# Optimization experiments

Hardware: AMD Instinct MI355X
Metric: run time of the kernel (lower is better)

## Reference

```python
import jax, jax.numpy as jnp
import numpy as np

EPS = 1e-5
ROPE_BASE = 10000.0

def _rms_norm(x, alpha):
    # var = eps + mean(x^2) (eps added to mean, matching _rms_norm)
    var = EPS + jnp.mean(x * x, axis=-1, keepdims=True)
    return x * (alpha * jax.lax.rsqrt(var))

def _rope(x, pos):
    # x: [B,H,T,D], pos: [T] absolute positions; interleaved pair rotation
    D = x.shape[-1]
    half = D // 2
    inv_freq = ROPE_BASE ** (-jnp.arange(half, dtype=x.dtype) / half)
    ang = pos.astype(x.dtype)[:, None] * inv_freq[None, :]          # [T,half]
    cos, sin = jnp.cos(ang), jnp.sin(ang)
    x1, x2 = x[..., ::2], x[..., 1::2]
    y1 = x1 * cos - x2 * sin
    y2 = x1 * sin + x2 * cos
    return jnp.stack([y1, y2], axis=-1).reshape(x.shape)

def setup_inputs() -> dict:
    key = jax.random.key(0)
    ks = jax.random.split(key, 9)
    B, T, C = 8, 256, 2048
    H, Dh, CAP, FF = 16, 128, 2048, 8192
    s = 0.02
    return {
        "x": jax.random.normal(ks[0], (B, T, C), jnp.float32),
        "kcache": jax.random.normal(ks[1], (B, H, CAP, Dh), jnp.float32) * s,
        "vcache": jax.random.normal(ks[2], (B, H, CAP, Dh), jnp.float32) * s,
        "in_proj_w": jax.random.normal(ks[3], (3 * C, C), jnp.float32) * s,
        "out_proj_w": jax.random.normal(ks[4], (C, C), jnp.float32) * s,
        "norm1_a": jnp.ones((C,), jnp.float32),
        "norm2_a": jnp.ones((C,), jnp.float32),
        "w1": jax.random.normal(ks[5], (FF, C), jnp.float32) * s,
        "w2": jax.random.normal(ks[6], (C, FF), jnp.float32) * s,
        "offset": 1024,
    }

def reference(x, kcache, vcache, in_proj_w, out_proj_w, norm1_a, norm2_a, w1, w2, offset):
    B, T, C = x.shape
    H = 16
    Dh = C // H
    CAP = kcache.shape[2]
    scale = 1.0 / np.sqrt(Dh)

    # ---- self-attention branch ----
    xn = _rms_norm(x, norm1_a)
    qkv = jnp.einsum('btc,oc->bto', xn, in_proj_w)                  # [B,T,3C]
    q, k, v = jnp.split(qkv, 3, axis=-1)
    def heads(t):  # [B,T,C] -> [B,H,T,Dh]
        return t.reshape(B, T, H, Dh).transpose(0, 2, 1, 3)
    q, k, v = heads(q), heads(k), heads(v)

    t_abs = offset + jnp.arange(T)                                   # absolute positions
    q = _rope(q, t_abs)
    k = _rope(k, t_abs)

    # ---- ring KV cache write: idx = (offset + t) % capacity ----
    widx = (offset + jnp.arange(T)) % CAP                            # [T]
    kcache = kcache.at[:, :, widx, :].set(k)
    vcache = vcache.at[:, :, widx, :].set(v)

    # ---- recover absolute positions of cache slots (RingKVCache.complete) ----
    idx = jnp.arange(CAP)
    last = offset + T - 1
    end_index = last % CAP
    delta = idx - end_index
    pos = jnp.where(delta <= 0, last + delta, last + delta - CAP)    # [CAP]
    invalid = idx >= (offset + T)
    pos = jnp.where(invalid, -1, pos)

    # ---- causal + context masked attention over full cache ----
    qpos = offset + jnp.arange(T)                                    # [T]
    d = qpos[:, None] - pos[None, :]                                 # [T,CAP]
    mask = (pos[None, :] >= 0) & (d >= 0) & (d < CAP)
    scores = jnp.einsum('bhtd,bhsd->bhts', q, kcache) * scale        # [B,H,T,CAP]
    scores = jnp.where(mask[None, None], scores, jnp.float32(-1e9))
    attn = jax.nn.softmax(scores, axis=-1)
    o = jnp.einsum('bhts,bhsd->bhtd', attn, vcache)                  # [B,H,T,Dh]
    o = o.transpose(0, 2, 1, 3).reshape(B, T, C)
    x = x + jnp.einsum('btc,oc->bto', o, out_proj_w)

    # ---- MLP branch ----
    h = _rms_norm(x, norm2_a)
    h = jax.nn.gelu(jnp.einsum('btc,fc->btf', h, w1), approximate=False)
    x = x + jnp.einsum('btf,cf->btc', h, w2)
    return x
```

## Files before the change

kernel.cpp:

```cpp
#include <hip/hip_runtime.h>
#include <math.h>


typedef __bf16 bf16_t;
typedef __bf16 bf16x8 __attribute__((ext_vector_type(8)));
typedef float  f32x4  __attribute__((ext_vector_type(4)));

#define MFMA(a, b, c) __builtin_amdgcn_mfma_f32_16x16x32_bf16((a), (b), (c), 0, 0, 0)

static __device__ __forceinline__ bf16x8 cvt8(const float* __restrict__ src) {
    f32x4 f0 = *(const f32x4*)src;
    f32x4 f1 = *(const f32x4*)(src + 4);
    bf16x8 v;
    v[0] = (bf16_t)f0[0]; v[1] = (bf16_t)f0[1]; v[2] = (bf16_t)f0[2]; v[3] = (bf16_t)f0[3];
    v[4] = (bf16_t)f1[0]; v[5] = (bf16_t)f1[1]; v[6] = (bf16_t)f1[2]; v[7] = (bf16_t)f1[3];
    return v;
}

static __device__ __forceinline__ void gload16(const bf16_t* g, bf16_t* lds) {
    __builtin_amdgcn_global_load_lds(
        (const __attribute__((address_space(1))) void*)g,
        (__attribute__((address_space(3))) void*)lds, 16, 0, 0);
}

__global__ __launch_bounds__(256)
void cvt_rows_kernel(const float* __restrict__ src, bf16_t* __restrict__ dst,
                     int cols, int src_stride)
{
    const int row = blockIdx.x;
    const float* s = src + (size_t)row * src_stride;
    bf16_t* d = dst + (size_t)row * cols;
    for (int c = threadIdx.x * 8; c < cols; c += blockDim.x * 8)
        *(bf16x8*)&d[c] = cvt8(&s[c]);
}

__global__ __launch_bounds__(256)
void rmsnorm_kernel(const float* __restrict__ x, const float* __restrict__ alpha,
                    bf16_t* __restrict__ out)
{
    const int C = 2048;
    const int row = blockIdx.x;
    const int tid = threadIdx.x;
    const float* xr = x + (size_t)row * C;
    f32x4 a0 = *(const f32x4*)&xr[tid * 8];
    f32x4 a1 = *(const f32x4*)&xr[tid * 8 + 4];
    float ss = a0[0]*a0[0] + a0[1]*a0[1] + a0[2]*a0[2] + a0[3]*a0[3]
             + a1[0]*a1[0] + a1[1]*a1[1] + a1[2]*a1[2] + a1[3]*a1[3];
    #pragma unroll
    for (int d = 32; d >= 1; d >>= 1) ss += __shfl_xor(ss, d);
    __shared__ float red[4];
    const int lane = tid & 63, wid = tid >> 6;
    if (lane == 0) red[wid] = ss;
    __syncthreads();
    const float tot = red[0] + red[1] + red[2] + red[3];
    const float rs = rsqrtf(1e-5f + tot * (1.0f / C));
    f32x4 l0 = *(const f32x4*)&alpha[tid * 8];
    f32x4 l1 = *(const f32x4*)&alpha[tid * 8 + 4];
    bf16x8 o8;
    o8[0] = (bf16_t)(a0[0] * l0[0] * rs); o8[1] = (bf16_t)(a0[1] * l0[1] * rs);
    o8[2] = (bf16_t)(a0[2] * l0[2] * rs); o8[3] = (bf16_t)(a0[3] * l0[3] * rs);
    o8[4] = (bf16_t)(a1[0] * l1[0] * rs); o8[5] = (bf16_t)(a1[1] * l1[1] * rs);
    o8[6] = (bf16_t)(a1[2] * l1[2] * rs); o8[7] = (bf16_t)(a1[3] * l1[3] * rs);
    *(bf16x8*)&out[(size_t)row * C + tid * 8] = o8;
}

template<int EPI, int NSPLIT>
__global__ __launch_bounds__(256)
void gemm_bb(const bf16_t* __restrict__ A, const bf16_t* __restrict__ B,
             float* Cf, bf16_t* Cb, const float* __restrict__ res,
             int M, int N, int K, int lda, int ldb)
{
    __shared__ bf16_t As[2][128 * 64];
    __shared__ bf16_t Bs[2][128 * 64];
    if constexpr (NSPLIT > 1) {
        A  += (size_t)blockIdx.z * K;
        B  += (size_t)blockIdx.z * K;
        Cb += (size_t)blockIdx.z * (size_t)M * N;
    }
    const int gx = gridDim.x;
    const int orig = blockIdx.y * gx + blockIdx.x;
    const int xcd = orig & 7;
    const int i = orig >> 3;
    const int bw = gx >> 3;
    const int m0 = (i / bw) * 128;
    const int n0 = (xcd * bw + (i % bw)) * 128;

    const int tid = threadIdx.x;
    const int lane = tid & 63, wid = tid >> 6;
    const int wr = wid >> 1, wc = wid & 1;
    const int lr = lane & 15, lg = lane >> 4;
    const int srow = lane >> 3;
    const int scol_swz = (((lane & 7) ^ (lane >> 3)) << 3);
    f32x4 acc[4][4] = {};

    const int nt = K >> 6;
    const bf16_t* Ab = A + (size_t)m0 * lda;
    const bf16_t* Bb = B + (size_t)n0 * ldb;

    #define STAGE(bufi, kt)                                                               \
        _Pragma("unroll")                                                                 \
        for (int it = 0; it < 4; ++it) {                                                  \
            const int r = wid * 32 + it * 8;                                              \
            gload16(&Ab[(size_t)(r + srow) * lda + (kt) + scol_swz], &As[bufi][r * 64]);  \
            gload16(&Bb[(size_t)(r + srow) * ldb + (kt) + scol_swz], &Bs[bufi][r * 64]);  \
        }

    STAGE(0, 0);
    __syncthreads();
    int cur = 0;
    for (int t = 0; t < nt; ++t) {
        if (t + 1 < nt) STAGE(cur ^ 1, (t + 1) << 6);
        __builtin_amdgcn_s_setprio(1);
        #pragma unroll
        for (int kk = 0; kk < 2; ++kk) {
            bf16x8 af[4], bfr[4];
            #pragma unroll
            for (int m = 0; m < 4; ++m)
                af[m] = *(const bf16x8*)&As[cur][(wr * 64 + m * 16 + lr) * 64
                                                 + (((kk * 4 + lg) ^ (lr & 7)) << 3)];
            #pragma unroll
            for (int n = 0; n < 4; ++n)
                bfr[n] = *(const bf16x8*)&Bs[cur][(wc * 64 + n * 16 + lr) * 64
                                                  + (((kk * 4 + lg) ^ (lr & 7)) << 3)];
            #pragma unroll
            for (int m = 0; m < 4; ++m)
                #pragma unroll
                for (int n = 0; n < 4; ++n)
                    acc[m][n] = MFMA(af[m], bfr[n], acc[m][n]);
        }
        __builtin_amdgcn_s_setprio(0);
        __syncthreads();
        cur ^= 1;
    }
    #undef STAGE

    #pragma unroll
    for (int m = 0; m < 4; ++m) {
        #pragma unroll
        for (int n = 0; n < 4; ++n) {
            const int gmb = m0 + wr * 64 + m * 16 + lg * 4;
            const int gn  = n0 + wc * 64 + n * 16 + lr;
            #pragma unroll
            for (int r = 0; r < 4; ++r) {
                const size_t off = (size_t)(gmb + r) * N + gn;
                const float v = acc[m][n][r];
                if (EPI == 0)      Cf[off] = v;
                else if (EPI == 1) Cf[off] = res[off] + v;
                else if (EPI == 2) Cb[off] = (bf16_t)(0.5f * v * (1.0f + erff(v * 0.70710678118654752f)));
                else               Cb[off] = (bf16_t)v;
            }
        }
    }
}

template<int Z>
__global__ __launch_bounds__(256)
void reduce_sk_kernel(const bf16_t* __restrict__ p, const float* __restrict__ res,
                      float* __restrict__ out, int n)
{
    for (int i = (blockIdx.x * 256 + threadIdx.x) * 8; i < n; i += gridDim.x * 256 * 8) {
        f32x4 r0 = *(const f32x4*)&res[i];
        f32x4 r1 = *(const f32x4*)&res[i + 4];
        #pragma unroll
        for (int z = 0; z < Z; ++z) {
            bf16x8 v = *(const bf16x8*)&p[(size_t)z * n + i];
            r0[0] += (float)v[0]; r0[1] += (float)v[1]; r0[2] += (float)v[2]; r0[3] += (float)v[3];
            r1[0] += (float)v[4]; r1[1] += (float)v[5]; r1[2] += (float)v[6]; r1[3] += (float)v[7];
        }
        *(f32x4*)&out[i] = r0;
        *(f32x4*)&out[i + 4] = r1;
    }
}

__global__ __launch_bounds__(256)
void rope_split_kernel(const bf16_t* __restrict__ qkv,
                       bf16_t* __restrict__ q, bf16_t* __restrict__ kn,
                       bf16_t* __restrict__ vn, const int* __restrict__ offp)
{
    const int m = blockIdx.x;
    const int b = m >> 8, t = m & 255;
    const int tid = threadIdx.x;
    const int c = tid * 8;
    const int h = c >> 7, d0 = c & 127;
    const int pos = offp[0] + t;
    bf16x8 qv = *(const bf16x8*)&qkv[(size_t)m * 6144 + c];
    bf16x8 kv = *(const bf16x8*)&qkv[(size_t)m * 6144 + 2048 + c];
    bf16x8 vv = *(const bf16x8*)&qkv[(size_t)m * 6144 + 4096 + c];
    bf16x8 qo, ko;
    #pragma unroll
    for (int p = 0; p < 4; ++p) {
        const int i = (d0 >> 1) + p;
        const float ang = (float)pos * __expf(-(float)i * 0.14391156861538527f);
        const float sn = sinf(ang), cs = cosf(ang);
        const float q1 = (float)qv[2 * p], q2 = (float)qv[2 * p + 1];
        const float k1 = (float)kv[2 * p], k2 = (float)kv[2 * p + 1];
        qo[2 * p]     = (bf16_t)(q1 * cs - q2 * sn);
        qo[2 * p + 1] = (bf16_t)(q1 * sn + q2 * cs);
        ko[2 * p]     = (bf16_t)(k1 * cs - k2 * sn);
        ko[2 * p + 1] = (bf16_t)(k1 * sn + k2 * cs);
    }
    const size_t oi = (((size_t)(b * 16 + h) * 256) + t) * 128 + d0;
    *(bf16x8*)&q[oi]  = qo;
    *(bf16x8*)&kn[oi] = ko;
    *(bf16x8*)&vn[oi] = vv;
}

__global__ __launch_bounds__(256)
void attn_kernel(const bf16_t* __restrict__ qh, const bf16_t* __restrict__ kn,
                 const bf16_t* __restrict__ vn, const float* __restrict__ kcache,
                 const float* __restrict__ vcache, bf16_t* __restrict__ outp,
                 const int* __restrict__ offp)
{
    const int T = 256, Dh = 128, CAP = 2048, H = 16;
    const float scale = 0.08838834764831845f;
    __shared__ bf16_t Ks[64][136];
    __shared__ bf16_t VtL[128 * 64];
    __shared__ bf16_t Pl[4][16][72];
    const int bh = blockIdx.x;
    const int t0 = blockIdx.y * 64;
    const int b = bh >> 4, h = bh & 15;
    const int offset = offp[0];
    const int Stot = offset + T;
    const int tid = threadIdx.x, lane = tid & 63, wid = tid >> 6;
    const int lr = lane & 15, lg = lane >> 4;

    bf16x8 qf[4];
    {
        const bf16_t* qbase = qh + ((size_t)bh * T + t0 + wid * 16) * Dh;
        #pragma unroll
        for (int ks = 0; ks < 4; ++ks)
            qf[ks] = *(const bf16x8*)&qbase[lr * Dh + ks * 32 + lg * 8];
    }
    f32x4 accO[8] = {};
    float mrun[4], lrun[4];
    #pragma unroll
    for (int r = 0; r < 4; ++r) { mrun[r] = -3e38f; lrun[r] = 0.0f; }

    int smax = offset + t0 + 64; if (smax > Stot) smax = Stot;
    const int nch = (smax + 63) >> 6;

    for (int ch = 0; ch < nch; ++ch) {
        const int s0 = ch * 64;
        __syncthreads();
        #pragma unroll
        for (int it = 0; it < 4; ++it) {
            const int idx = tid + it * 256;
            const int r = idx >> 4, c8 = idx & 15;
            const int s = s0 + r;
            bf16x8 kv8, vv8;
            if (s < offset) {
                const size_t base = (((size_t)b * H + h) * CAP + s) * Dh + c8 * 8;
                kv8 = cvt8(&kcache[base]);
                vv8 = cvt8(&vcache[base]);
            } else if (s < Stot) {
                const size_t base = ((size_t)bh * T + (s - offset)) * Dh + c8 * 8;
                kv8 = *(const bf16x8*)&kn[base];
                vv8 = *(const bf16x8*)&vn[base];
            } else {
                #pragma unroll
                for (int j = 0; j < 8; ++j) { kv8[j] = (bf16_t)0.0f; vv8[j] = (bf16_t)0.0f; }
            }
            *(bf16x8*)&Ks[r][c8 * 8] = kv8;
            #pragma unroll
            for (int j = 0; j < 8; ++j)
                VtL[(c8 * 8 + j) * 64 + ((((r >> 3) ^ j ^ (c8 & 7))) << 3) + (r & 7)] = vv8[j];
        }
        __syncthreads();

        f32x4 sc[4] = {};
        #pragma unroll
        for (int ks = 0; ks < 4; ++ks) {
            bf16x8 kf[4];
            #pragma unroll
            for (int n = 0; n < 4; ++n)
                kf[n] = *(const bf16x8*)&Ks[n * 16 + lr][ks * 32 + lg * 8];
            #pragma unroll
            for (int n = 0; n < 4; ++n)
                sc[n] = MFMA(qf[ks], kf[n], sc[n]);
        }

        #pragma unroll
        for (int r = 0; r < 4; ++r) {
            const int qpos = offset + t0 + wid * 16 + lg * 4 + r;
            float mx = -3e38f;
            #pragma unroll
            for (int n = 0; n < 4; ++n) {
                const int sabs = s0 + n * 16 + lr;
                float v = sc[n][r] * scale;
                v = (sabs <= qpos && sabs < Stot) ? v : -1e30f;
                sc[n][r] = v;
                mx = fmaxf(mx, v);
            }
            #pragma unroll
            for (int d = 8; d >= 1; d >>= 1) mx = fmaxf(mx, __shfl_xor(mx, d));
            const float mo = mrun[r];
            const float mn2 = fmaxf(mo, mx);
            const float al = __expf(mo - mn2);
            mrun[r] = mn2;
            lrun[r] *= al;
            #pragma unroll
            for (int df = 0; df < 8; ++df) accO[df][r] *= al;
            float rsum = 0.0f;
            #pragma unroll
            for (int n = 0; n < 4; ++n) {
                const float p = __expf(sc[n][r] - mn2);
                sc[n][r] = p;
                rsum += p;
            }
            #pragma unroll
            for (int d = 8; d >= 1; d >>= 1) rsum += __shfl_xor(rsum, d);
            lrun[r] += rsum;
            #pragma unroll
            for (int n = 0; n < 4; ++n)
                Pl[wid][lg * 4 + r][n * 16 + lr] = (bf16_t)sc[n][r];
        }
        asm volatile("s_waitcnt lgkmcnt(0)" ::: "memory");
        __builtin_amdgcn_sched_barrier(0);

        #pragma unroll
        for (int ks2 = 0; ks2 < 2; ++ks2) {
            const bf16x8 pa = *(const bf16x8*)&Pl[wid][lr][ks2 * 32 + lg * 8];
            #pragma unroll
            for (int df = 0; df < 8; ++df) {
                const int d = df * 16 + lr;
                const bf16x8 vb8 = *(const bf16x8*)
                    &VtL[d * 64 + (((ks2 * 4 + lg) ^ (d & 7) ^ ((d >> 3) & 7)) << 3)];
                accO[df] = MFMA(pa, vb8, accO[df]);
            }
        }
    }

    float rinv[4];
    #pragma unroll
    for (int r = 0; r < 4; ++r) rinv[r] = 1.0f / lrun[r];
    #pragma unroll
    for (int df = 0; df < 8; ++df) {
        #pragma unroll
        for (int r = 0; r < 4; ++r) {
            const int t = t0 + wid * 16 + lg * 4 + r;
            outp[((size_t)b * 256 + t) * 2048 + h * 128 + df * 16 + lr] =
                (bf16_t)(accO[df][r] * rinv[r]);
        }
    }
}

extern "C" void kernel_launch(void* const* d_in, const int* in_sizes, int n_in,
                              void* d_out, int out_size, void* d_ws, size_t ws_size,
                              hipStream_t stream)
{
    const float* x    = (const float*)d_in[0];
    const float* kc   = (const float*)d_in[1];
    const float* vc   = (const float*)d_in[2];
    const float* wqkv = (const float*)d_in[3];
    const float* wo   = (const float*)d_in[4];
    const float* a1   = (const float*)d_in[5];
    const float* a2   = (const float*)d_in[6];
    const float* w1   = (const float*)d_in[7];
    const float* w2   = (const float*)d_in[8];
    const int*   offp = (const int*)d_in[9];
    float* out = (float*)d_out;

    char* ws = (char*)d_ws;
    bf16_t* xn     = (bf16_t*)(ws + 0);
    bf16_t* wqkv_b = (bf16_t*)(ws + (8ull  << 20));
    bf16_t* qkv    = (bf16_t*)(ws + (32ull << 20));
    bf16_t* q      = (bf16_t*)(ws + (8ull  << 20));
    bf16_t* kn     = (bf16_t*)(ws + (16ull << 20));
    bf16_t* vn     = (bf16_t*)(ws + (24ull << 20));
    bf16_t* wo_b   = (bf16_t*)(ws + (32ull << 20));
    bf16_t* o      = (bf16_t*)(ws + (40ull << 20));
    bf16_t* oprt   = (bf16_t*)(ws + (48ull << 20));
    bf16_t* hbuf   = (bf16_t*)(ws + 0);
    const bool bigws = ws_size >= (137ull << 20);

    rmsnorm_kernel<<<2048, 256, 0, stream>>>(x, a1, xn);
    cvt_rows_kernel<<<6144, 256, 0, stream>>>(wqkv, wqkv_b, 2048, 2048);
    gemm_bb<3, 1><<<dim3(48, 16), 256, 0, stream>>>(xn, wqkv_b, nullptr, qkv, nullptr,
                                                    2048, 6144, 2048, 2048, 2048);
    rope_split_kernel<<<2048, 256, 0, stream>>>(qkv, q, kn, vn, offp);
    cvt_rows_kernel<<<2048, 256, 0, stream>>>(wo, wo_b, 2048, 2048);
    attn_kernel<<<dim3(128, 4), 256, 0, stream>>>(q, kn, vn, kc, vc, o, offp);
    gemm_bb<3, 2><<<dim3(16, 16, 2), 256, 0, stream>>>(o, wo_b, nullptr, oprt, nullptr,
                                                       2048, 2048, 1024, 2048, 2048);
    reduce_sk_kernel<2><<<2048, 256, 0, stream>>>(oprt, x, out, 2048 * 2048);
    rmsnorm_kernel<<<2048, 256, 0, stream>>>(out, a2, hbuf);

    if (bigws) {
        bf16_t* w1b = (bf16_t*)(ws + (8ull   << 20));
        bf16_t* g   = (bf16_t*)(ws + (40ull  << 20));
        bf16_t* w2b = (bf16_t*)(ws + (72ull  << 20));
        bf16_t* prt = (bf16_t*)(ws + (104ull << 20));
        cvt_rows_kernel<<<8192, 256, 0, stream>>>(w1, w1b, 2048, 2048);
        gemm_bb<2, 1><<<dim3(64, 16), 256, 0, stream>>>(hbuf, w1b, nullptr, g, nullptr,
                                                        2048, 8192, 2048, 2048, 2048);
        cvt_rows_kernel<<<2048, 256, 0, stream>>>(w2, w2b, 8192, 8192);
        gemm_bb<3, 4><<<dim3(16, 16, 4), 256, 0, stream>>>(g, w2b, nullptr, prt, nullptr,
                                                           2048, 2048, 2048, 8192, 8192);
        reduce_sk_kernel<4><<<2048, 256, 0, stream>>>(prt, out, out, 2048 * 2048);
    } else {
        bf16_t* w1b = (bf16_t*)(ws + (8ull  << 20));
        bf16_t* g_h = (bf16_t*)(ws + (24ull << 20));
        bf16_t* w2b = (bf16_t*)(ws + (40ull << 20));
        bf16_t* prt = (bf16_t*)(ws + (8ull  << 20));
        for (int hh = 0; hh < 2; ++hh) {
            cvt_rows_kernel<<<4096, 256, 0, stream>>>(w1 + (size_t)hh * 4096 * 2048, w1b, 2048, 2048);
            gemm_bb<2, 1><<<dim3(32, 16), 256, 0, stream>>>(hbuf, w1b, nullptr, g_h, nullptr,
                                                            2048, 4096, 2048, 2048, 2048);
            cvt_rows_kernel<<<2048, 256, 0, stream>>>(w2 + (size_t)hh * 4096, w2b, 4096, 8192);
            gemm_bb<3, 2><<<dim3(16, 16, 2), 256, 0, stream>>>(g_h, w2b, nullptr, prt, nullptr,
                                                               2048, 2048, 2048, 4096, 4096);
            reduce_sk_kernel<2><<<2048, 256, 0, stream>>>(prt, out, out, 2048 * 2048);
        }
    }
}
```

Before: 445.8 us.

## Double-buffer attention KV chunks with register prefetch of next chunk

The attention kernel now issues global loads for the next 64-row K/V chunk into registers before computing on the current chunk, then converts and writes them into a second LDS buffer on the next iteration. The aim is to hide global-memory latency behind the QK and PV MFMA work. It also adds a launch-bounds occupancy hint of 2 blocks per CU. In exchange it doubles LDS for K/V and holds 16 extra f32x4 registers per thread, which may raise register pressure or cause spills.

Measured after the change: 495.7 us. 11.2% more time.

```diff
diff --git a/kernel.cpp b/kernel.cpp
--- a/kernel.cpp
+++ b/kernel.cpp
@@ -11,6 +11,13 @@
 static __device__ __forceinline__ bf16x8 cvt8(const float* __restrict__ src) {
     f32x4 f0 = *(const f32x4*)src;
     f32x4 f1 = *(const f32x4*)(src + 4);
+    bf16x8 v;
+    v[0] = (bf16_t)f0[0]; v[1] = (bf16_t)f0[1]; v[2] = (bf16_t)f0[2]; v[3] = (bf16_t)f0[3];
+    v[4] = (bf16_t)f1[0]; v[5] = (bf16_t)f1[1]; v[6] = (bf16_t)f1[2]; v[7] = (bf16_t)f1[3];
+    return v;
+}
+
+static __device__ __forceinline__ bf16x8 cvt8r(f32x4 f0, f32x4 f1) {
     bf16x8 v;
     v[0] = (bf16_t)f0[0]; v[1] = (bf16_t)f0[1]; v[2] = (bf16_t)f0[2]; v[3] = (bf16_t)f0[3];
     v[4] = (bf16_t)f1[0]; v[5] = (bf16_t)f1[1]; v[6] = (bf16_t)f1[2]; v[7] = (bf16_t)f1[3];
@@ -205,7 +212,7 @@
     *(bf16x8*)&vn[oi] = vv;
 }
 
-__global__ __launch_bounds__(256)
+__global__ __launch_bounds__(256, 2)
 void attn_kernel(const bf16_t* __restrict__ qh, const bf16_t* __restrict__ kn,
                  const bf16_t* __restrict__ vn, const float* __restrict__ kcache,
                  const float* __restrict__ vcache, bf16_t* __restrict__ outp,
@@ -213,8 +220,8 @@
 {
     const int T = 256, Dh = 128, CAP = 2048, H = 16;
     const float scale = 0.08838834764831845f;
-    __shared__ bf16_t Ks[64][136];
-    __shared__ bf16_t VtL[128 * 64];
+    __shared__ bf16_t Ks[2][64][136];
+    __shared__ bf16_t VtL[2][128 * 64];
     __shared__ bf16_t Pl[4][16][72];
     const int bh = blockIdx.x;
     const int t0 = blockIdx.y * 64;
@@ -239,9 +246,28 @@
     int smax = offset + t0 + 64; if (smax > Stot) smax = Stot;
     const int nch = (smax + 63) >> 6;
 
-    for (int ch = 0; ch < nch; ++ch) {
-        const int s0 = ch * 64;
-        __syncthreads();
+    f32x4 ka[4], kb[4], va[4], vb[4];
+
+    auto LOADCH = [&](int s0) {
+        #pragma unroll
+        for (int it = 0; it < 4; ++it) {
+            const int idx = tid + it * 256;
+            const int r = idx >> 4, c8 = idx & 15;
+            const int s = s0 + r;
+            if (s < offset) {
+                const size_t base = (((size_t)b * H + h) * CAP + s) * Dh + c8 * 8;
+                ka[it] = *(const f32x4*)&kcache[base];
+                kb[it] = *(const f32x4*)&kcache[base + 4];
+                va[it] = *(const f32x4*)&vcache[base];
+                vb[it] = *(const f32x4*)&vcache[base + 4];
+            } else if (s < Stot) {
+                const size_t base = ((size_t)bh * T + (s - offset)) * Dh + c8 * 8;
+                ka[it] = __builtin_bit_cast(f32x4, *(const bf16x8*)&kn[base]);
+                va[it] = __builtin_bit_cast(f32x4, *(const bf16x8*)&vn[base]);
+            }
+        }
+    };
+    auto WRITECH = [&](int bufi, int s0) {
         #pragma unroll
         for (int it = 0; it < 4; ++it) {
             const int idx = tid + it * 256;
@@ -249,23 +275,29 @@
             const int s = s0 + r;
             bf16x8 kv8, vv8;
             if (s < offset) {
-                const size_t base = (((size_t)b * H + h) * CAP + s) * Dh + c8 * 8;
-                kv8 = cvt8(&kcache[base]);
-                vv8 = cvt8(&vcache[base]);
+                kv8 = cvt8r(ka[it], kb[it]);
+                vv8 = cvt8r(va[it], vb[it]);
             } else if (s < Stot) {
-                const size_t base = ((size_t)bh * T + (s - offset)) * Dh + c8 * 8;
-                kv8 = *(const bf16x8*)&kn[base];
-                vv8 = *(const bf16x8*)&vn[base];
+                kv8 = __builtin_bit_cast(bf16x8, ka[it]);
+                vv8 = __builtin_bit_cast(bf16x8, va[it]);
             } else {
                 #pragma unroll
                 for (int j = 0; j < 8; ++j) { kv8[j] = (bf16_t)0.0f; vv8[j] = (bf16_t)0.0f; }
             }
-            *(bf16x8*)&Ks[r][c8 * 8] = kv8;
+            *(bf16x8*)&Ks[bufi][r][c8 * 8] = kv8;
             #pragma unroll
             for (int j = 0; j < 8; ++j)
-                VtL[(c8 * 8 + j) * 64 + ((((r >> 3) ^ j ^ (c8 & 7))) << 3) + (r & 7)] = vv8[j];
-        }
+                VtL[bufi][(c8 * 8 + j) * 64 + ((((r >> 3) ^ j ^ (c8 & 7))) << 3) + (r & 7)] = vv8[j];
+        }
+    };
+
+    LOADCH(0);
+    int cur = 0;
+    for (int ch = 0; ch < nch; ++ch) {
+        const int s0 = ch * 64;
+        WRITECH(cur, s0);
         __syncthreads();
+        if (ch + 1 < nch) LOADCH(s0 + 64);
 
         f32x4 sc[4] = {};
         #pragma unroll
@@ -273,7 +305,7 @@
             bf16x8 kf[4];
             #pragma unroll
             for (int n = 0; n < 4; ++n)
-                kf[n] = *(const bf16x8*)&Ks[n * 16 + lr][ks * 32 + lg * 8];
+                kf[n] = *(const bf16x8*)&Ks[cur][n * 16 + lr][ks * 32 + lg * 8];
             #pragma unroll
             for (int n = 0; n < 4; ++n)
                 sc[n] = MFMA(qf[ks], kf[n], sc[n]);
@@ -324,10 +356,11 @@
             for (int df = 0; df < 8; ++df) {
                 const int d = df * 16 + lr;
                 const bf16x8 vb8 = *(const bf16x8*)
-                    &VtL[d * 64 + (((ks2 * 4 + lg) ^ (d & 7) ^ ((d >> 3) & 7)) << 3)];
+                    &VtL[cur][d * 64 + (((ks2 * 4 + lg) ^ (d & 7) ^ ((d >> 3) & 7)) << 3)];
                 accO[df] = MFMA(pa, vb8, accO[df]);
             }
         }
+        cur ^= 1;
     }
 
     float rinv[4];
```

## Split attention KV chunks across two blocks with a flash-decoding combine

Applied to the files above, without the earlier changes.

The attention kernel now launches twice as many blocks, and each one handles alternating 64-key chunks of the cache. Each block writes an unnormalized partial output plus its running max and sum, and a new combine kernel merges the two halves with log-sum-exp weights. The aim is more parallelism, since only 512 blocks originally ran long serial loops over up to 1280 keys. In exchange it adds an extra kernel launch, bf16 partial-output traffic, and rounding of the unnormalized accumulators to bf16.

After: 455.6 us. 2.2% more time.

```diff
diff --git a/kernel.cpp b/kernel.cpp
--- a/kernel.cpp
+++ b/kernel.cpp
@@ -208,7 +208,8 @@
 __global__ __launch_bounds__(256)
 void attn_kernel(const bf16_t* __restrict__ qh, const bf16_t* __restrict__ kn,
                  const bf16_t* __restrict__ vn, const float* __restrict__ kcache,
-                 const float* __restrict__ vcache, bf16_t* __restrict__ outp,
+                 const float* __restrict__ vcache,
+                 bf16_t* __restrict__ Opart, float* __restrict__ mlbuf,
                  const int* __restrict__ offp)
 {
     const int T = 256, Dh = 128, CAP = 2048, H = 16;
@@ -217,12 +218,15 @@
     __shared__ bf16_t VtL[128 * 64];
     __shared__ bf16_t Pl[4][16][72];
     const int bh = blockIdx.x;
-    const int t0 = blockIdx.y * 64;
+    const int tt = blockIdx.y;
+    const int par = blockIdx.z;
+    const int t0 = tt * 64;
     const int b = bh >> 4, h = bh & 15;
     const int offset = offp[0];
     const int Stot = offset + T;
     const int tid = threadIdx.x, lane = tid & 63, wid = tid >> 6;
     const int lr = lane & 15, lg = lane >> 4;
+    const int tile2 = (bh * 4 + tt) * 2 + par;
 
     bf16x8 qf[4];
     {
@@ -239,7 +243,7 @@
     int smax = offset + t0 + 64; if (smax > Stot) smax = Stot;
     const int nch = (smax + 63) >> 6;
 
-    for (int ch = 0; ch < nch; ++ch) {
+    for (int ch = par; ch < nch; ch += 2) {
         const int s0 = ch * 64;
         __syncthreads();
         #pragma unroll
@@ -330,17 +334,52 @@
         }
     }
 
-    float rinv[4];
-    #pragma unroll
-    for (int r = 0; r < 4; ++r) rinv[r] = 1.0f / lrun[r];
-    #pragma unroll
-    for (int df = 0; df < 8; ++df) {
+    const size_t obase = (size_t)tile2 * 64 * 128;
+    #pragma unroll
+    for (int df = 0; df < 8; ++df)
         #pragma unroll
         for (int r = 0; r < 4; ++r) {
-            const int t = t0 + wid * 16 + lg * 4 + r;
-            outp[((size_t)b * 256 + t) * 2048 + h * 128 + df * 16 + lr] =
-                (bf16_t)(accO[df][r] * rinv[r]);
-        }
+            const int row = wid * 16 + lg * 4 + r;
+            Opart[obase + (size_t)row * 128 + df * 16 + lr] = (bf16_t)accO[df][r];
+        }
+    if (lr == 0) {
+        #pragma unroll
+        for (int r = 0; r < 4; ++r) {
+            const int row = wid * 16 + lg * 4 + r;
+            mlbuf[(size_t)tile2 * 128 + row]      = mrun[r];
+            mlbuf[(size_t)tile2 * 128 + 64 + row] = lrun[r];
+        }
+    }
+}
+
+__global__ __launch_bounds__(256)
+void attn_combine_kernel(const bf16_t* __restrict__ Op, const float* __restrict__ ml,
+                         bf16_t* __restrict__ outp)
+{
+    const int tile = blockIdx.x;
+    const int bh = tile >> 2, tt = tile & 3;
+    const int b = bh >> 4, h = bh & 15;
+    const int row = threadIdx.x >> 2;
+    const int d0 = (threadIdx.x & 3) * 32;
+    const int t20 = tile * 2, t21 = tile * 2 + 1;
+    const float m0 = ml[(size_t)t20 * 128 + row], l0 = ml[(size_t)t20 * 128 + 64 + row];
+    const float m1 = ml[(size_t)t21 * 128 + row], l1 = ml[(size_t)t21 * 128 + 64 + row];
+    const float mm = fmaxf(m0, m1);
+    const float w0 = __expf(m0 - mm), w1 = __expf(m1 - mm);
+    const float den = l0 * w0 + l1 * w1;
+    const float s0 = w0 / den, s1 = w1 / den;
+    const size_t b0 = (size_t)t20 * 8192 + (size_t)row * 128 + d0;
+    const size_t b1 = (size_t)t21 * 8192 + (size_t)row * 128 + d0;
+    const int t = tt * 64 + row;
+    bf16_t* op = &outp[((size_t)b * 256 + t) * 2048 + h * 128 + d0];
+    #pragma unroll
+    for (int j = 0; j < 4; ++j) {
+        bf16x8 a = *(const bf16x8*)&Op[b0 + j * 8];
+        bf16x8 c = *(const bf16x8*)&Op[b1 + j * 8];
+        bf16x8 o;
+        #pragma unroll
+        for (int e = 0; e < 8; ++e) o[e] = (bf16_t)((float)a[e] * s0 + (float)c[e] * s1);
+        *(bf16x8*)&op[j * 8] = o;
     }
 }
 
@@ -364,11 +403,13 @@
     bf16_t* xn     = (bf16_t*)(ws + 0);
     bf16_t* wqkv_b = (bf16_t*)(ws + (8ull  << 20));
     bf16_t* qkv    = (bf16_t*)(ws + (32ull << 20));
+    float*  mlbuf  = (float*) (ws + 0);
     bf16_t* q      = (bf16_t*)(ws + (8ull  << 20));
     bf16_t* kn     = (bf16_t*)(ws + (16ull << 20));
     bf16_t* vn     = (bf16_t*)(ws + (24ull << 20));
     bf16_t* wo_b   = (bf16_t*)(ws + (32ull << 20));
     bf16_t* o      = (bf16_t*)(ws + (40ull << 20));
+    bf16_t* Opart  = (bf16_t*)(ws + (48ull << 20));
     bf16_t* oprt   = (bf16_t*)(ws + (48ull << 20));
     bf16_t* hbuf   = (bf16_t*)(ws + 0);
     const bool bigws = ws_size >= (137ull << 20);
@@ -379,7 +420,8 @@
                                                     2048, 6144, 2048, 2048, 2048);
     rope_split_kernel<<<2048, 256, 0, stream>>>(qkv, q, kn, vn, offp);
     cvt_rows_kernel<<<2048, 256, 0, stream>>>(wo, wo_b, 2048, 2048);
-    attn_kernel<<<dim3(128, 4), 256, 0, stream>>>(q, kn, vn, kc, vc, o, offp);
+    attn_kernel<<<dim3(128, 4, 2), 256, 0, stream>>>(q, kn, vn, kc, vc, Opart, mlbuf, offp);
+    attn_combine_kernel<<<512, 256, 0, stream>>>(Opart, mlbuf, o);
     gemm_bb<3, 2><<<dim3(16, 16, 2), 256, 0, stream>>>(o, wo_b, nullptr, oprt, nullptr,
                                                        2048, 2048, 1024, 2048, 2048);
     reduce_sk_kernel<2><<<2048, 256, 0, stream>>>(oprt, x, out, 2048 * 2048);
```
